# Optimization experiments

Hardware: AMD Instinct MI355X
Metric: run time of the kernel (lower is better)

## Reference

```python
import jax, jax.numpy as jnp
import numpy as np

B, IN, P, H, OUT = 131072, 40, 128, 256, 1

def setup_inputs() -> dict:
    key = jax.random.key(0)
    ks = jax.random.split(key, 10)
    s_in, s_h = 1.0 / np.sqrt(IN), 1.0 / np.sqrt(H)
    return {
        "x_step": jax.random.normal(ks[0], (B, 1, IN), jnp.float32),
        "hidden_in": jax.random.normal(ks[1], (1, B, H), jnp.float32),
        "W_proj": jax.random.uniform(ks[2], (P, IN), jnp.float32, -s_in, s_in),
        "b_proj": jax.random.uniform(ks[3], (P,), jnp.float32, -s_in, s_in),
        "W_ih": jax.random.uniform(ks[4], (3 * H, P), jnp.float32, -s_h, s_h),
        "W_hh": jax.random.uniform(ks[5], (3 * H, H), jnp.float32, -s_h, s_h),
        "b_ih": jax.random.uniform(ks[6], (3 * H,), jnp.float32, -s_h, s_h),
        "b_hh": jax.random.uniform(ks[7], (3 * H,), jnp.float32, -s_h, s_h),
        "W_head": jax.random.uniform(ks[8], (OUT, H), jnp.float32, -s_h, s_h),
        "b_head": jax.random.uniform(ks[9], (OUT,), jnp.float32, -s_h, s_h),
    }

def reference(x_step, hidden_in, W_proj, b_proj, W_ih, W_hh, b_ih, b_hh, W_head, b_head):
    # input projection: [B,1,IN] -> [B,P]
    x = jnp.einsum('bi,pi->bp', x_step[:, 0, :], W_proj) + b_proj
    h = hidden_in[0]  # [B,H]
    # single GRU step (PyTorch gate layout: reset, update, new)
    gi = jnp.einsum('bp,gp->bg', x, W_ih) + b_ih  # [B,3H]
    gh = jnp.einsum('bh,gh->bg', h, W_hh) + b_hh  # [B,3H]
    i_r, i_z, i_n = jnp.split(gi, 3, axis=-1)
    h_r, h_z, h_n = jnp.split(gh, 3, axis=-1)
    r = jax.nn.sigmoid(i_r + h_r)
    z = jax.nn.sigmoid(i_z + h_z)
    n = jnp.tanh(i_n + r * h_n)
    h_new = (1.0 - z) * n + z * h  # [B,H]
    pred = jnp.einsum('bh,oh->bo', h_new, W_head) + b_head  # [B,OUT]
    return pred[:, None, :], h_new[None]  # ([B,1,OUT], [1,B,H])
```

## Files before the change

kernel.cpp:

```cpp
#include <hip/hip_runtime.h>

#define B_N 131072
#define IN_N 40
#define H_N 256

typedef __bf16 bf16x8 __attribute__((ext_vector_type(8)));
typedef __bf16 bf16x4 __attribute__((ext_vector_type(4)));
typedef float f32x4 __attribute__((ext_vector_type(4)));

#define MFMA(a, b, c) __builtin_amdgcn_mfma_f32_16x16x32_bf16(a, b, c, 0, 0, 0)

#define WSF 0
#define WSH 49152
#define WSBI 245760
#define PREP_N (245760 + 768 + B_N)

__global__ void prep(const float* __restrict__ Wp, const float* __restrict__ bp,
                     const float* __restrict__ Wih, const float* __restrict__ Whh,
                     const float* __restrict__ bih, const float* __restrict__ bhead,
                     __bf16* __restrict__ wsb, float* __restrict__ out) {
  int i = blockIdx.x * 256 + threadIdx.x;
  if (i < WSH) {
    int g = i >> 6, kk = i & 63;
    float v = 0.f;
    if (kk < IN_N) {
      for (int p = 0; p < 128; ++p) v += Wih[g * 128 + p] * Wp[p * IN_N + kk];
    }
    wsb[i] = (__bf16)v;
  } else if (i < WSBI) {
    wsb[i] = (__bf16)Whh[i - WSH];
  } else if (i < WSBI + 768) {
    int g = i - WSBI;
    float v = bih[g];
    for (int p = 0; p < 128; ++p) v += Wih[g * 128 + p] * bp[p];
    ((float*)(wsb + WSBI))[g] = v;
  } else if (i < PREP_N) {
    out[i - (WSBI + 768)] = bhead[0];
  }
}

__global__ __launch_bounds__(512, 2) void gru_v6(
    const float* __restrict__ x, const float* __restrict__ h0,
    const __bf16* __restrict__ wsb, const float* __restrict__ bhh,
    const float* __restrict__ Whead, float* __restrict__ out) {
  __shared__ __bf16 hs[2][64][264];
  __shared__ __bf16 xs[2][64][72];

  const int tid = threadIdx.x;
  const int lane = tid & 63;
  const int w = tid >> 6;
  const int l15 = lane & 15;
  const int l4 = lane >> 4;
  const int koff = l4 * 8;

  const int b = blockIdx.x;
  const int v = (b & 7) * 64 + (b >> 3);
  const int half = v & 1;
  const int tile0 = (v >> 1) * 8;
  const int col = half * 128 + w * 16 + l15;

  const __bf16* WH = wsb + WSH;
  const __bf16* WF = wsb + WSF;
  bf16x8 whR[8], whZ[8], whN[8], wfR[2], wfZ[2], wfN[2];
#pragma unroll
  for (int ks = 0; ks < 8; ++ks) {
    const int k = ks * 32 + koff;
    whR[ks] = *reinterpret_cast<const bf16x8*>(WH + (size_t)col * 256 + k);
    whZ[ks] = *reinterpret_cast<const bf16x8*>(WH + (size_t)(256 + col) * 256 + k);
    whN[ks] = *reinterpret_cast<const bf16x8*>(WH + (size_t)(512 + col) * 256 + k);
  }
#pragma unroll
  for (int ks = 0; ks < 2; ++ks) {
    const int k = ks * 32 + koff;
    wfR[ks] = *reinterpret_cast<const bf16x8*>(WF + (size_t)col * 64 + k);
    wfZ[ks] = *reinterpret_cast<const bf16x8*>(WF + (size_t)(256 + col) * 64 + k);
    wfN[ks] = *reinterpret_cast<const bf16x8*>(WF + (size_t)(512 + col) * 64 + k);
  }
  const float* bfused = (const float*)(wsb + WSBI);
  const float bR = bfused[col] + bhh[col];
  const float bZ = bfused[256 + col] + bhh[256 + col];
  const float bI = bfused[512 + col];
  const float bH = bhh[512 + col];
  const float whead = Whead[col];

  auto stage = [&](int buf, int row0) {
    const float* hb = h0 + (size_t)row0 * H_N;
#pragma unroll
    for (int j = 0; j < 8; ++j) {
      const int flat = (tid + j * 512) * 4;
      const int r = flat >> 8, c = flat & 255;
      float4 vv = *reinterpret_cast<const float4*>(hb + flat);
      bf16x4 u;
      u[0] = (__bf16)vv.x; u[1] = (__bf16)vv.y; u[2] = (__bf16)vv.z; u[3] = (__bf16)vv.w;
      *reinterpret_cast<bf16x4*>(&hs[buf][r][c]) = u;
    }
    const float* xb = x + (size_t)row0 * IN_N;
#pragma unroll
    for (int j = 0; j < 5; ++j) {
      const int i = tid + j * 512;
      xs[buf][i / 40][i % 40] = (__bf16)xb[i];
    }
#pragma unroll
    for (int j = 0; j < 3; ++j) {
      const int i = tid + j * 512;
      xs[buf][i / 24][40 + i % 24] = (__bf16)0.f;
    }
  };

  stage(0, tile0 * 64);
  __syncthreads();

  for (int t = 0; t < 8; ++t) {
    const int cur = t & 1;
    const int row0 = (tile0 + t) * 64;
    if (t < 7) stage(cur ^ 1, row0 + 64);

    f32x4 aR[4], aZ[4], aI[4], aH[4];
#pragma unroll
    for (int mi = 0; mi < 4; ++mi) {
      aR[mi] = (f32x4){bR, bR, bR, bR};
      aZ[mi] = (f32x4){bZ, bZ, bZ, bZ};
      aI[mi] = (f32x4){bI, bI, bI, bI};
      aH[mi] = (f32x4){bH, bH, bH, bH};
    }
#pragma unroll
    for (int ks = 0; ks < 2; ++ks) {
#pragma unroll
      for (int mi = 0; mi < 4; ++mi) {
        const bf16x8 a = *reinterpret_cast<const bf16x8*>(&xs[cur][mi * 16 + l15][ks * 32 + koff]);
        aR[mi] = MFMA(a, wfR[ks], aR[mi]);
        aZ[mi] = MFMA(a, wfZ[ks], aZ[mi]);
        aI[mi] = MFMA(a, wfN[ks], aI[mi]);
      }
    }
#pragma unroll
    for (int ks = 0; ks < 8; ++ks) {
#pragma unroll
      for (int mi = 0; mi < 4; ++mi) {
        const bf16x8 a = *reinterpret_cast<const bf16x8*>(&hs[cur][mi * 16 + l15][ks * 32 + koff]);
        aR[mi] = MFMA(a, whR[ks], aR[mi]);
        aZ[mi] = MFMA(a, whZ[ks], aZ[mi]);
        aH[mi] = MFMA(a, whN[ks], aH[mi]);
      }
    }
    float ps[4][4];
#pragma unroll
    for (int mi = 0; mi < 4; ++mi) {
#pragma unroll
      for (int r = 0; r < 4; ++r) {
        const int row = mi * 16 + l4 * 4 + r;
        const float rg = 1.f / (1.f + __expf(-aR[mi][r]));
        const float zg = 1.f / (1.f + __expf(-aZ[mi][r]));
        const float e2 = __expf(2.f * (aI[mi][r] + rg * aH[mi][r]));
        const float ng = (e2 - 1.f) / (e2 + 1.f);
        const float hv = (float)hs[cur][row][col];
        const float hn = (1.f - zg) * ng + zg * hv;
        out[(size_t)B_N + (size_t)(row0 + row) * H_N + col] = hn;
        ps[mi][r] = hn * whead;
      }
    }
#pragma unroll
    for (int mi = 0; mi < 4; ++mi)
#pragma unroll
      for (int r = 0; r < 4; ++r) {
        float s = ps[mi][r];
        s += __shfl_xor(s, 1);
        s += __shfl_xor(s, 2);
        s += __shfl_xor(s, 4);
        s += __shfl_xor(s, 8);
        if (l15 == 0) atomicAdd(&out[row0 + mi * 16 + l4 * 4 + r], s);
      }
    __syncthreads();
  }
}

extern "C" void kernel_launch(void* const* d_in, const int* in_sizes, int n_in,
                              void* d_out, int out_size, void* d_ws, size_t ws_size,
                              hipStream_t stream) {
  const float* x     = (const float*)d_in[0];
  const float* h0    = (const float*)d_in[1];
  const float* Wp    = (const float*)d_in[2];
  const float* bp    = (const float*)d_in[3];
  const float* Wih   = (const float*)d_in[4];
  const float* Whh   = (const float*)d_in[5];
  const float* bih   = (const float*)d_in[6];
  const float* bhh   = (const float*)d_in[7];
  const float* Whead = (const float*)d_in[8];
  const float* bhead = (const float*)d_in[9];
  float* out = (float*)d_out;
  __bf16* wsb = (__bf16*)d_ws;

  prep<<<(PREP_N + 255) / 256, 256, 0, stream>>>(Wp, bp, Wih, Whh, bih, bhead, wsb, out);
  gru_v6<<<512, 512, 0, stream>>>(x, h0, wsb, bhh, Whead, out);
}
```

Before: 216.2 us.

## Stream weights from global per k-step and pipeline h loads with MFMA

Replaces register-resident gate weights with a pre-swizzled weight layout streamed from global memory in double-buffered slots, interleaved with MFMA groups. Block shape changes to 256 threads covering 64 output columns, with 1024 blocks. Staging of h/x is split into register loads and later LDS writes spread across the compute, and LDS uses an XOR swizzle instead of padding. Also uses rcp intrinsics for the gates and batches the atomics. The aim is to cut register pressure and hide global load latency behind compute, at the cost of re-reading weights from L2 each tile and sending more atomics per row, since four blocks now contribute to each row instead of two.

```diff
diff --git a/kernel.cpp b/kernel.cpp
--- a/kernel.cpp
+++ b/kernel.cpp
@@ -5,13 +5,12 @@
 #define H_N 256
 
 typedef __bf16 bf16x8 __attribute__((ext_vector_type(8)));
-typedef __bf16 bf16x4 __attribute__((ext_vector_type(4)));
 typedef float f32x4 __attribute__((ext_vector_type(4)));
 
 #define MFMA(a, b, c) __builtin_amdgcn_mfma_f32_16x16x32_bf16(a, b, c, 0, 0, 0)
 
-#define WSF 0
-#define WSH 49152
+#define WSGH 0
+#define WSGI 196608
 #define WSBI 245760
 #define PREP_N (245760 + 768 + B_N)
 
@@ -20,15 +19,18 @@
                      const float* __restrict__ bih, const float* __restrict__ bhead,
                      __bf16* __restrict__ wsb, float* __restrict__ out) {
   int i = blockIdx.x * 256 + threadIdx.x;
-  if (i < WSH) {
-    int g = i >> 6, kk = i & 63;
+  if (i < WSGI) {
+    int e = i & 31, col = (i >> 5) & 255, ks = (i >> 13) & 7, g = i >> 16;
+    wsb[i] = (__bf16)Whh[(g * 256 + col) * 256 + ks * 32 + e];
+  } else if (i < WSBI) {
+    int j = i - WSGI;
+    int e = j & 31, col = (j >> 5) & 255, ks2 = (j >> 13) & 1, g = j >> 14;
+    int k = ks2 * 32 + e;
     float v = 0.f;
-    if (kk < IN_N) {
-      for (int p = 0; p < 128; ++p) v += Wih[g * 128 + p] * Wp[p * IN_N + kk];
+    if (k < IN_N) {
+      for (int p = 0; p < 128; ++p) v += Wih[(g * 256 + col) * 128 + p] * Wp[p * IN_N + k];
     }
     wsb[i] = (__bf16)v;
-  } else if (i < WSBI) {
-    wsb[i] = (__bf16)Whh[i - WSH];
   } else if (i < WSBI + 768) {
     int g = i - WSBI;
     float v = bih[g];
@@ -39,43 +41,30 @@
   }
 }
 
-__global__ __launch_bounds__(512, 2) void gru_v6(
+__global__ __launch_bounds__(256, 2) void gru_v7(
     const float* __restrict__ x, const float* __restrict__ h0,
     const __bf16* __restrict__ wsb, const float* __restrict__ bhh,
     const float* __restrict__ Whead, float* __restrict__ out) {
-  __shared__ __bf16 hs[2][64][264];
-  __shared__ __bf16 xs[2][64][72];
+  __shared__ __align__(16) __bf16 hs[2][64 * 256];
+  __shared__ __align__(16) __bf16 xs[64][72];
 
   const int tid = threadIdx.x;
   const int lane = tid & 63;
   const int w = tid >> 6;
   const int l15 = lane & 15;
   const int l4 = lane >> 4;
-  const int koff = l4 * 8;
 
   const int b = blockIdx.x;
-  const int v = (b & 7) * 64 + (b >> 3);
-  const int half = v & 1;
-  const int tile0 = (v >> 1) * 8;
-  const int col = half * 128 + w * 16 + l15;
-
-  const __bf16* WH = wsb + WSH;
-  const __bf16* WF = wsb + WSF;
-  bf16x8 whR[8], whZ[8], whN[8], wfR[2], wfZ[2], wfN[2];
-#pragma unroll
-  for (int ks = 0; ks < 8; ++ks) {
-    const int k = ks * 32 + koff;
-    whR[ks] = *reinterpret_cast<const bf16x8*>(WH + (size_t)col * 256 + k);
-    whZ[ks] = *reinterpret_cast<const bf16x8*>(WH + (size_t)(256 + col) * 256 + k);
-    whN[ks] = *reinterpret_cast<const bf16x8*>(WH + (size_t)(512 + col) * 256 + k);
-  }
-#pragma unroll
-  for (int ks = 0; ks < 2; ++ks) {
-    const int k = ks * 32 + koff;
-    wfR[ks] = *reinterpret_cast<const bf16x8*>(WF + (size_t)col * 64 + k);
-    wfZ[ks] = *reinterpret_cast<const bf16x8*>(WF + (size_t)(256 + col) * 64 + k);
-    wfN[ks] = *reinterpret_cast<const bf16x8*>(WF + (size_t)(512 + col) * 64 + k);
-  }
+  const int lin = (b & 7) * 128 + (b >> 3);
+  const int ch = lin & 3;
+  const int seg0 = (lin >> 2) * 8;
+
+  const int cb = ch * 64 + w * 16;
+  const int col = cb + l15;
+
+  const __bf16* lgh = wsb + WSGH + (size_t)(cb + l15) * 32 + l4 * 8;
+  const __bf16* lgi = wsb + WSGI + (size_t)(cb + l15) * 32 + l4 * 8;
+
   const float* bfused = (const float*)(wsb + WSBI);
   const float bR = bfused[col] + bhh[col];
   const float bZ = bfused[256 + col] + bhh[256 + col];
@@ -83,79 +72,137 @@
   const float bH = bhh[512 + col];
   const float whead = Whead[col];
 
-  auto stage = [&](int buf, int row0) {
-    const float* hb = h0 + (size_t)row0 * H_N;
-#pragma unroll
-    for (int j = 0; j < 8; ++j) {
-      const int flat = (tid + j * 512) * 4;
-      const int r = flat >> 8, c = flat & 255;
-      float4 vv = *reinterpret_cast<const float4*>(hb + flat);
-      bf16x4 u;
-      u[0] = (__bf16)vv.x; u[1] = (__bf16)vv.y; u[2] = (__bf16)vv.z; u[3] = (__bf16)vv.w;
-      *reinterpret_cast<bf16x4*>(&hs[buf][r][c]) = u;
-    }
-    const float* xb = x + (size_t)row0 * IN_N;
-#pragma unroll
-    for (int j = 0; j < 5; ++j) {
-      const int i = tid + j * 512;
-      xs[buf][i / 40][i % 40] = (__bf16)xb[i];
-    }
-#pragma unroll
-    for (int j = 0; j < 3; ++j) {
-      const int i = tid + j * 512;
-      xs[buf][i / 24][40 + i % 24] = (__bf16)0.f;
-    }
-  };
-
-  stage(0, tile0 * 64);
+  for (int j = tid; j < 64 * 24; j += 256) xs[j / 24][40 + j % 24] = (__bf16)0.f;
+
+  float4 svA[4], svB[4], xv[4];
+
+  auto loadH = [&](float4(&sv)[4], int seg, int q) {
+#pragma unroll
+    for (int kk = 0; kk < 2; ++kk) {
+      const int cid = tid + kk * 256;
+      const int rl = q * 16 + (cid >> 5), ck = cid & 31;
+      const float* src = h0 + ((size_t)seg * 64 + rl) * H_N + ck * 8;
+      sv[kk * 2] = *reinterpret_cast<const float4*>(src);
+      sv[kk * 2 + 1] = *reinterpret_cast<const float4*>(src + 4);
+    }
+  };
+  auto writeH = [&](float4(&sv)[4], int buf, int q) {
+#pragma unroll
+    for (int kk = 0; kk < 2; ++kk) {
+      const int cid = tid + kk * 256;
+      const int rl = q * 16 + (cid >> 5), ck = cid & 31;
+      bf16x8 u;
+      u[0] = (__bf16)sv[kk * 2].x; u[1] = (__bf16)sv[kk * 2].y;
+      u[2] = (__bf16)sv[kk * 2].z; u[3] = (__bf16)sv[kk * 2].w;
+      u[4] = (__bf16)sv[kk * 2 + 1].x; u[5] = (__bf16)sv[kk * 2 + 1].y;
+      u[6] = (__bf16)sv[kk * 2 + 1].z; u[7] = (__bf16)sv[kk * 2 + 1].w;
+      *reinterpret_cast<bf16x8*>(&hs[buf][rl * 256 + ((ck ^ (rl & 7)) << 3)]) = u;
+    }
+  };
+  auto loadX = [&](int seg) {
+    const int c0 = tid, c1 = 256 + (tid & 63);
+    const float* sx = x + (size_t)seg * 64 * IN_N;
+    xv[0] = *reinterpret_cast<const float4*>(sx + c0 * 8);
+    xv[1] = *reinterpret_cast<const float4*>(sx + c0 * 8 + 4);
+    xv[2] = *reinterpret_cast<const float4*>(sx + c1 * 8);
+    xv[3] = *reinterpret_cast<const float4*>(sx + c1 * 8 + 4);
+  };
+  auto writeX = [&]() {
+    const int c0 = tid, c1 = 256 + (tid & 63);
+    bf16x8 u0, u1;
+    u0[0] = (__bf16)xv[0].x; u0[1] = (__bf16)xv[0].y; u0[2] = (__bf16)xv[0].z; u0[3] = (__bf16)xv[0].w;
+    u0[4] = (__bf16)xv[1].x; u0[5] = (__bf16)xv[1].y; u0[6] = (__bf16)xv[1].z; u0[7] = (__bf16)xv[1].w;
+    u1[0] = (__bf16)xv[2].x; u1[1] = (__bf16)xv[2].y; u1[2] = (__bf16)xv[2].z; u1[3] = (__bf16)xv[2].w;
+    u1[4] = (__bf16)xv[3].x; u1[5] = (__bf16)xv[3].y; u1[6] = (__bf16)xv[3].z; u1[7] = (__bf16)xv[3].w;
+    *reinterpret_cast<bf16x8*>(&xs[c0 / 5][(c0 % 5) * 8]) = u0;
+    *reinterpret_cast<bf16x8*>(&xs[c1 / 5][(c1 % 5) * 8]) = u1;
+  };
+
+  bf16x8 wR[2], wZ[2], wN[2];
+  auto loadWgrp = [&](int slot, int grp) {
+    if (grp < 2) {
+      wR[slot] = *reinterpret_cast<const bf16x8*>(lgi + (0 * 2 + grp) * 8192);
+      wZ[slot] = *reinterpret_cast<const bf16x8*>(lgi + (1 * 2 + grp) * 8192);
+      wN[slot] = *reinterpret_cast<const bf16x8*>(lgi + (2 * 2 + grp) * 8192);
+    } else {
+      const int ks = grp - 2;
+      wR[slot] = *reinterpret_cast<const bf16x8*>(lgh + (0 * 8 + ks) * 8192);
+      wZ[slot] = *reinterpret_cast<const bf16x8*>(lgh + (1 * 8 + ks) * 8192);
+      wN[slot] = *reinterpret_cast<const bf16x8*>(lgh + (2 * 8 + ks) * 8192);
+    }
+  };
+
+  f32x4 aR4[4], aZ4[4], aI4[4], aH4[4];
+  auto grpGI = [&](int slot, int ks2) {
+#pragma unroll
+    for (int mi = 0; mi < 4; ++mi) {
+      const bf16x8 a = *reinterpret_cast<const bf16x8*>(&xs[mi * 16 + l15][ks2 * 32 + l4 * 8]);
+      aR4[mi] = MFMA(a, wR[slot], aR4[mi]);
+      aZ4[mi] = MFMA(a, wZ[slot], aZ4[mi]);
+      aI4[mi] = MFMA(a, wN[slot], aI4[mi]);
+    }
+  };
+  auto grpGH = [&](const __bf16* hb, int slot, int ks) {
+#pragma unroll
+    for (int mi = 0; mi < 4; ++mi) {
+      const int row = mi * 16 + l15;
+      const int ck = (ks * 4 + l4) ^ (row & 7);
+      const bf16x8 a = *reinterpret_cast<const bf16x8*>(&hb[row * 256 + ck * 8]);
+      aR4[mi] = MFMA(a, wR[slot], aR4[mi]);
+      aZ4[mi] = MFMA(a, wZ[slot], aZ4[mi]);
+      aH4[mi] = MFMA(a, wN[slot], aH4[mi]);
+    }
+  };
+
+  loadH(svA, seg0, 0); writeH(svA, 0, 0);
+  loadH(svA, seg0, 1); writeH(svA, 0, 1);
+  loadH(svA, seg0, 2); writeH(svA, 0, 2);
+  loadH(svA, seg0, 3); writeH(svA, 0, 3);
+  loadX(seg0); writeX();
+  loadWgrp(0, 0); loadWgrp(1, 1);
   __syncthreads();
 
   for (int t = 0; t < 8; ++t) {
     const int cur = t & 1;
-    const int row0 = (tile0 + t) * 64;
-    if (t < 7) stage(cur ^ 1, row0 + 64);
-
-    f32x4 aR[4], aZ[4], aI[4], aH[4];
-#pragma unroll
-    for (int mi = 0; mi < 4; ++mi) {
-      aR[mi] = (f32x4){bR, bR, bR, bR};
-      aZ[mi] = (f32x4){bZ, bZ, bZ, bZ};
-      aI[mi] = (f32x4){bI, bI, bI, bI};
-      aH[mi] = (f32x4){bH, bH, bH, bH};
-    }
-#pragma unroll
-    for (int ks = 0; ks < 2; ++ks) {
-#pragma unroll
-      for (int mi = 0; mi < 4; ++mi) {
-        const bf16x8 a = *reinterpret_cast<const bf16x8*>(&xs[cur][mi * 16 + l15][ks * 32 + koff]);
-        aR[mi] = MFMA(a, wfR[ks], aR[mi]);
-        aZ[mi] = MFMA(a, wfZ[ks], aZ[mi]);
-        aI[mi] = MFMA(a, wfN[ks], aI[mi]);
-      }
-    }
-#pragma unroll
-    for (int ks = 0; ks < 8; ++ks) {
-#pragma unroll
-      for (int mi = 0; mi < 4; ++mi) {
-        const bf16x8 a = *reinterpret_cast<const bf16x8*>(&hs[cur][mi * 16 + l15][ks * 32 + koff]);
-        aR[mi] = MFMA(a, whR[ks], aR[mi]);
-        aZ[mi] = MFMA(a, whZ[ks], aZ[mi]);
-        aH[mi] = MFMA(a, whN[ks], aH[mi]);
-      }
-    }
+    const int seg = seg0 + t;
+    const int nseg = (t < 7) ? seg + 1 : seg;
+    const __bf16* hb = hs[cur];
+
+#pragma unroll
+    for (int mi = 0; mi < 4; ++mi) {
+      aR4[mi] = (f32x4){bR, bR, bR, bR};
+      aZ4[mi] = (f32x4){bZ, bZ, bZ, bZ};
+      aI4[mi] = (f32x4){bI, bI, bI, bI};
+      aH4[mi] = (f32x4){bH, bH, bH, bH};
+    }
+
+    grpGI(0, 0); loadWgrp(0, 2);
+    grpGI(1, 1); loadWgrp(1, 3);
+    __syncthreads();
+
+    grpGH(hb, 0, 0); loadWgrp(0, 4); loadH(svA, nseg, 0);
+    grpGH(hb, 1, 1); loadWgrp(1, 5); loadH(svB, nseg, 1);
+    grpGH(hb, 0, 2); loadWgrp(0, 6);
+    grpGH(hb, 1, 3); loadWgrp(1, 7); writeH(svA, cur ^ 1, 0); loadH(svA, nseg, 2);
+    grpGH(hb, 0, 4); loadWgrp(0, 8); writeH(svB, cur ^ 1, 1); loadH(svB, nseg, 3);
+    grpGH(hb, 1, 5); loadWgrp(1, 9); loadX(nseg);
+    grpGH(hb, 0, 6); loadWgrp(0, 0); writeH(svA, cur ^ 1, 2);
+    grpGH(hb, 1, 7); loadWgrp(1, 1); writeH(svB, cur ^ 1, 3); writeX();
+
     float ps[4][4];
 #pragma unroll
     for (int mi = 0; mi < 4; ++mi) {
 #pragma unroll
       for (int r = 0; r < 4; ++r) {
         const int row = mi * 16 + l4 * 4 + r;
-        const float rg = 1.f / (1.f + __expf(-aR[mi][r]));
-        const float zg = 1.f / (1.f + __expf(-aZ[mi][r]));
-        const float e2 = __expf(2.f * (aI[mi][r] + rg * aH[mi][r]));
-        const float ng = (e2 - 1.f) / (e2 + 1.f);
-        const float hv = (float)hs[cur][row][col];
+        const float rg = __builtin_amdgcn_rcpf(1.f + __expf(-aR4[mi][r]));
+        const float zg = __builtin_amdgcn_rcpf(1.f + __expf(-aZ4[mi][r]));
+        const float e2 = __expf(2.f * (aI4[mi][r] + rg * aH4[mi][r]));
+        const float ng = 1.f - 2.f * __builtin_amdgcn_rcpf(e2 + 1.f);
+        const int ckv = (col >> 3) ^ (row & 7);
+        const float hv = (float)hb[row * 256 + ckv * 8 + (col & 7)];
         const float hn = (1.f - zg) * ng + zg * hv;
-        out[(size_t)B_N + (size_t)(row0 + row) * H_N + col] = hn;
+        out[(size_t)B_N + ((size_t)seg * 64 + row) * H_N + col] = hn;
         ps[mi][r] = hn * whead;
       }
     }
@@ -168,8 +215,15 @@
         s += __shfl_xor(s, 2);
         s += __shfl_xor(s, 4);
         s += __shfl_xor(s, 8);
-        if (l15 == 0) atomicAdd(&out[row0 + mi * 16 + l4 * 4 + r], s);
+        ps[mi][r] = s;
       }
+    if (l15 == 0) {
+#pragma unroll
+      for (int mi = 0; mi < 4; ++mi)
+#pragma unroll
+        for (int r = 0; r < 4; ++r)
+          atomicAdd(&out[seg * 64 + mi * 16 + l4 * 4 + r], ps[mi][r]);
+    }
     __syncthreads();
   }
 }
@@ -191,5 +245,5 @@
   __bf16* wsb = (__bf16*)d_ws;
 
   prep<<<(PREP_N + 255) / 256, 256, 0, stream>>>(Wp, bp, Wih, Whh, bih, bhead, wsb, out);
-  gru_v6<<<512, 512, 0, stream>>>(x, h0, wsb, bhh, Whead, out);
+  gru_v7<<<1024, 256, 0, stream>>>(x, h0, wsb, bhh, Whead, out);
 }
```

Result: slower. 284.1 us (+31.4%).

## Replace persistent register-resident weight kernel with many small blocks streaming fragment-packed weights

Applied to the files above, without the earlier changes.

Drops the persistent kernel that held weights in registers and looped over eight double-buffered 64-row tiles per block. The new kernel launches 8192 blocks of 256 threads; each handles one 64-row batch tile and a quarter of the hidden columns, loading weight fragments from a prepacked, coalesced layout built by the prep kernel. It relies on block-level parallelism and occupancy instead of in-block pipelining. Each h/x row tile is now staged four times (once per column quarter), and weights are re-read from L2 by every block.

```diff
diff --git a/kernel.cpp b/kernel.cpp
--- a/kernel.cpp
+++ b/kernel.cpp
@@ -5,13 +5,12 @@
 #define H_N 256
 
 typedef __bf16 bf16x8 __attribute__((ext_vector_type(8)));
-typedef __bf16 bf16x4 __attribute__((ext_vector_type(4)));
 typedef float f32x4 __attribute__((ext_vector_type(4)));
 
 #define MFMA(a, b, c) __builtin_amdgcn_mfma_f32_16x16x32_bf16(a, b, c, 0, 0, 0)
 
-#define WSF 0
-#define WSH 49152
+#define WSGH 0
+#define WSGI 196608
 #define WSBI 245760
 #define PREP_N (245760 + 768 + B_N)
 
@@ -20,15 +19,18 @@
                      const float* __restrict__ bih, const float* __restrict__ bhead,
                      __bf16* __restrict__ wsb, float* __restrict__ out) {
   int i = blockIdx.x * 256 + threadIdx.x;
-  if (i < WSH) {
-    int g = i >> 6, kk = i & 63;
+  if (i < WSGI) {
+    int e = i & 31, col = (i >> 5) & 255, ks = (i >> 13) & 7, g = i >> 16;
+    wsb[i] = (__bf16)Whh[(g * 256 + col) * 256 + ks * 32 + e];
+  } else if (i < WSBI) {
+    int j = i - WSGI;
+    int e = j & 31, col = (j >> 5) & 255, ks2 = (j >> 13) & 1, g = j >> 14;
+    int k = ks2 * 32 + e;
     float v = 0.f;
-    if (kk < IN_N) {
-      for (int p = 0; p < 128; ++p) v += Wih[g * 128 + p] * Wp[p * IN_N + kk];
+    if (k < IN_N) {
+      for (int p = 0; p < 128; ++p) v += Wih[(g * 256 + col) * 128 + p] * Wp[p * IN_N + k];
     }
     wsb[i] = (__bf16)v;
-  } else if (i < WSBI) {
-    wsb[i] = (__bf16)Whh[i - WSH];
   } else if (i < WSBI + 768) {
     int g = i - WSBI;
     float v = bih[g];
@@ -39,12 +41,12 @@
   }
 }
 
-__global__ __launch_bounds__(512, 2) void gru_v6(
+__global__ __launch_bounds__(256, 3) void gru_v8(
     const float* __restrict__ x, const float* __restrict__ h0,
     const __bf16* __restrict__ wsb, const float* __restrict__ bhh,
     const float* __restrict__ Whead, float* __restrict__ out) {
-  __shared__ __bf16 hs[2][64][264];
-  __shared__ __bf16 xs[2][64][72];
+  __shared__ __align__(16) __bf16 hs[64][264];
+  __shared__ __align__(16) __bf16 xs[64][72];
 
   const int tid = threadIdx.x;
   const int lane = tid & 63;
@@ -53,29 +55,42 @@
   const int l4 = lane >> 4;
   const int koff = l4 * 8;
 
-  const int b = blockIdx.x;
-  const int v = (b & 7) * 64 + (b >> 3);
-  const int half = v & 1;
-  const int tile0 = (v >> 1) * 8;
-  const int col = half * 128 + w * 16 + l15;
+  const int lin = (blockIdx.x & 7) * 1024 + (blockIdx.x >> 3);
+  const int ch = lin & 3;
+  const int b0 = (lin >> 2) * 64;
+  const int col = ch * 64 + w * 16 + l15;
 
-  const __bf16* WH = wsb + WSH;
-  const __bf16* WF = wsb + WSF;
-  bf16x8 whR[8], whZ[8], whN[8], wfR[2], wfZ[2], wfN[2];
+  for (int j = tid; j < 64 * 24; j += 256) xs[j / 24][40 + j % 24] = (__bf16)0.f;
 #pragma unroll
-  for (int ks = 0; ks < 8; ++ks) {
-    const int k = ks * 32 + koff;
-    whR[ks] = *reinterpret_cast<const bf16x8*>(WH + (size_t)col * 256 + k);
-    whZ[ks] = *reinterpret_cast<const bf16x8*>(WH + (size_t)(256 + col) * 256 + k);
-    whN[ks] = *reinterpret_cast<const bf16x8*>(WH + (size_t)(512 + col) * 256 + k);
+  for (int j = 0; j < 2; ++j) {
+    const int cid = tid + j * 256;
+    if (cid < 320) {
+      const int r = cid / 5, cc = cid % 5;
+      const float* s = x + (size_t)(b0 + r) * IN_N + cc * 8;
+      const float4 a = *reinterpret_cast<const float4*>(s);
+      const float4 b = *reinterpret_cast<const float4*>(s + 4);
+      bf16x8 u;
+      u[0] = (__bf16)a.x; u[1] = (__bf16)a.y; u[2] = (__bf16)a.z; u[3] = (__bf16)a.w;
+      u[4] = (__bf16)b.x; u[5] = (__bf16)b.y; u[6] = (__bf16)b.z; u[7] = (__bf16)b.w;
+      *reinterpret_cast<bf16x8*>(&xs[r][cc * 8]) = u;
+    }
   }
 #pragma unroll
-  for (int ks = 0; ks < 2; ++ks) {
-    const int k = ks * 32 + koff;
-    wfR[ks] = *reinterpret_cast<const bf16x8*>(WF + (size_t)col * 64 + k);
-    wfZ[ks] = *reinterpret_cast<const bf16x8*>(WF + (size_t)(256 + col) * 64 + k);
-    wfN[ks] = *reinterpret_cast<const bf16x8*>(WF + (size_t)(512 + col) * 64 + k);
+  for (int j = 0; j < 8; ++j) {
+    const int cid = tid + j * 256;
+    const int r = cid >> 5, cc = cid & 31;
+    const float* s = h0 + (size_t)(b0 + r) * H_N + cc * 8;
+    const float4 a = *reinterpret_cast<const float4*>(s);
+    const float4 b = *reinterpret_cast<const float4*>(s + 4);
+    bf16x8 u;
+    u[0] = (__bf16)a.x; u[1] = (__bf16)a.y; u[2] = (__bf16)a.z; u[3] = (__bf16)a.w;
+    u[4] = (__bf16)b.x; u[5] = (__bf16)b.y; u[6] = (__bf16)b.z; u[7] = (__bf16)b.w;
+    *reinterpret_cast<bf16x8*>(&hs[r][cc * 8]) = u;
   }
+  __syncthreads();
+
+  const __bf16* lgh = wsb + WSGH + (size_t)col * 32 + koff;
+  const __bf16* lgi = wsb + WSGI + (size_t)col * 32 + koff;
   const float* bfused = (const float*)(wsb + WSBI);
   const float bR = bfused[col] + bhh[col];
   const float bZ = bfused[256 + col] + bhh[256 + col];
@@ -83,95 +98,69 @@
   const float bH = bhh[512 + col];
   const float whead = Whead[col];
 
-  auto stage = [&](int buf, int row0) {
-    const float* hb = h0 + (size_t)row0 * H_N;
+  f32x4 aR[4], aZ[4], aI[4], aH[4];
 #pragma unroll
-    for (int j = 0; j < 8; ++j) {
-      const int flat = (tid + j * 512) * 4;
-      const int r = flat >> 8, c = flat & 255;
-      float4 vv = *reinterpret_cast<const float4*>(hb + flat);
-      bf16x4 u;
-      u[0] = (__bf16)vv.x; u[1] = (__bf16)vv.y; u[2] = (__bf16)vv.z; u[3] = (__bf16)vv.w;
-      *reinterpret_cast<bf16x4*>(&hs[buf][r][c]) = u;
-    }
-    const float* xb = x + (size_t)row0 * IN_N;
+  for (int mi = 0; mi < 4; ++mi) {
+    aR[mi] = (f32x4){bR, bR, bR, bR};
+    aZ[mi] = (f32x4){bZ, bZ, bZ, bZ};
+    aI[mi] = (f32x4){bI, bI, bI, bI};
+    aH[mi] = (f32x4){bH, bH, bH, bH};
+  }
+
 #pragma unroll
-    for (int j = 0; j < 5; ++j) {
-      const int i = tid + j * 512;
-      xs[buf][i / 40][i % 40] = (__bf16)xb[i];
-    }
-#pragma unroll
-    for (int j = 0; j < 3; ++j) {
-      const int i = tid + j * 512;
-      xs[buf][i / 24][40 + i % 24] = (__bf16)0.f;
-    }
-  };
-
-  stage(0, tile0 * 64);
-  __syncthreads();
-
-  for (int t = 0; t < 8; ++t) {
-    const int cur = t & 1;
-    const int row0 = (tile0 + t) * 64;
-    if (t < 7) stage(cur ^ 1, row0 + 64);
-
-    f32x4 aR[4], aZ[4], aI[4], aH[4];
+  for (int ks = 0; ks < 2; ++ks) {
+    const bf16x8 wR = *reinterpret_cast<const bf16x8*>(lgi + (0 * 2 + ks) * 8192);
+    const bf16x8 wZ = *reinterpret_cast<const bf16x8*>(lgi + (1 * 2 + ks) * 8192);
+    const bf16x8 wN = *reinterpret_cast<const bf16x8*>(lgi + (2 * 2 + ks) * 8192);
 #pragma unroll
     for (int mi = 0; mi < 4; ++mi) {
-      aR[mi] = (f32x4){bR, bR, bR, bR};
-      aZ[mi] = (f32x4){bZ, bZ, bZ, bZ};
-      aI[mi] = (f32x4){bI, bI, bI, bI};
-      aH[mi] = (f32x4){bH, bH, bH, bH};
+      const bf16x8 a = *reinterpret_cast<const bf16x8*>(&xs[mi * 16 + l15][ks * 32 + koff]);
+      aR[mi] = MFMA(a, wR, aR[mi]);
+      aZ[mi] = MFMA(a, wZ, aZ[mi]);
+      aI[mi] = MFMA(a, wN, aI[mi]);
     }
+  }
 #pragma unroll
-    for (int ks = 0; ks < 2; ++ks) {
-#pragma unroll
-      for (int mi = 0; mi < 4; ++mi) {
-        const bf16x8 a = *reinterpret_cast<const bf16x8*>(&xs[cur][mi * 16 + l15][ks * 32 + koff]);
-        aR[mi] = MFMA(a, wfR[ks], aR[mi]);
-        aZ[mi] = MFMA(a, wfZ[ks], aZ[mi]);
-        aI[mi] = MFMA(a, wfN[ks], aI[mi]);
-      }
-    }
-#pragma unroll
-    for (int ks = 0; ks < 8; ++ks) {
-#pragma unroll
-      for (int mi = 0; mi < 4; ++mi) {
-        const bf16x8 a = *reinterpret_cast<const bf16x8*>(&hs[cur][mi * 16 + l15][ks * 32 + koff]);
-        aR[mi] = MFMA(a, whR[ks], aR[mi]);
-        aZ[mi] = MFMA(a, whZ[ks], aZ[mi]);
-        aH[mi] = MFMA(a, whN[ks], aH[mi]);
-      }
-    }
-    float ps[4][4];
+  for (int ks = 0; ks < 8; ++ks) {
+    const bf16x8 wR = *reinterpret_cast<const bf16x8*>(lgh + (0 * 8 + ks) * 8192);
+    const bf16x8 wZ = *reinterpret_cast<const bf16x8*>(lgh + (1 * 8 + ks) * 8192);
+    const bf16x8 wN = *reinterpret_cast<const bf16x8*>(lgh + (2 * 8 + ks) * 8192);
 #pragma unroll
     for (int mi = 0; mi < 4; ++mi) {
+      const bf16x8 a = *reinterpret_cast<const bf16x8*>(&hs[mi * 16 + l15][ks * 32 + koff]);
+      aR[mi] = MFMA(a, wR, aR[mi]);
+      aZ[mi] = MFMA(a, wZ, aZ[mi]);
+      aH[mi] = MFMA(a, wN, aH[mi]);
+    }
+  }
+
+  float ps[4][4];
 #pragma unroll
-      for (int r = 0; r < 4; ++r) {
-        const int row = mi * 16 + l4 * 4 + r;
-        const float rg = 1.f / (1.f + __expf(-aR[mi][r]));
-        const float zg = 1.f / (1.f + __expf(-aZ[mi][r]));
-        const float e2 = __expf(2.f * (aI[mi][r] + rg * aH[mi][r]));
-        const float ng = (e2 - 1.f) / (e2 + 1.f);
-        const float hv = (float)hs[cur][row][col];
-        const float hn = (1.f - zg) * ng + zg * hv;
-        out[(size_t)B_N + (size_t)(row0 + row) * H_N + col] = hn;
-        ps[mi][r] = hn * whead;
-      }
+  for (int mi = 0; mi < 4; ++mi) {
+#pragma unroll
+    for (int r = 0; r < 4; ++r) {
+      const int row = mi * 16 + l4 * 4 + r;
+      const float rg = 1.f / (1.f + __expf(-aR[mi][r]));
+      const float zg = 1.f / (1.f + __expf(-aZ[mi][r]));
+      const float e2 = __expf(2.f * (aI[mi][r] + rg * aH[mi][r]));
+      const float ng = (e2 - 1.f) / (e2 + 1.f);
+      const float hv = (float)hs[row][col];
+      const float hn = (1.f - zg) * ng + zg * hv;
+      out[(size_t)B_N + (size_t)(b0 + row) * H_N + col] = hn;
+      ps[mi][r] = hn * whead;
     }
+  }
 #pragma unroll
-    for (int mi = 0; mi < 4; ++mi)
+  for (int mi = 0; mi < 4; ++mi)
 #pragma unroll
-      for (int r = 0; r < 4; ++r) {
-        float s = ps[mi][r];
-        s += __shfl_xor(s, 1);
-        s += __shfl_xor(s, 2);
-        s += __shfl_xor(s, 4);
-        s += __shfl_xor(s, 8);
-        if (l15 == 0) atomicAdd(&out[row0 + mi * 16 + l4 * 4 + r], s);
-      }
-    __syncthreads();
-  }
+    for (int r = 0; r < 4; ++r) {
+      float s = ps[mi][r];
+      s += __shfl_xor(s, 1);
+      s += __shfl_xor(s, 2);
+      s += __shfl_xor(s, 4);
+      s += __shfl_xor(s, 8);
+      if (l15 == 0) atomicAdd(&out[b0 + mi * 16 + l4 * 4 + r], s);
+    }
 }
 
 extern "C" void kernel_launch(void* const* d_in, const int* in_sizes, int n_in,
@@ -191,5 +180,5 @@
   __bf16* wsb = (__bf16*)d_ws;
 
   prep<<<(PREP_N + 255) / 256, 256, 0, stream>>>(Wp, bp, Wih, Whh, bih, bhead, wsb, out);
-  gru_v6<<<512, 512, 0, stream>>>(x, h0, wsb, bhh, Whead, out);
+  gru_v8<<<8192, 256, 0, stream>>>(x, h0, wsb, bhh, Whead, out);
 }
```

Result: slower. 251.9 us (+16.5%).

## Prefetch next tile into registers during MFMA and relayout weights for coalescing

Applied to the files above, without the earlier changes.

The next tile's h and x loads are now issued into registers before the MFMA loop and written to shared memory after it, so global latency overlaps the matrix math instead of stalling ahead of it. Prep now stores the weights in a ks-major, column-interleaved layout so each lane's weight fragment loads are contiguous across lanes. The zero padding of xs is written once up front rather than every iteration, and launch bounds drop from 2 to 1 blocks per SM. The larger register footprint from prefetching and the lower occupancy hint could reduce latency hiding.

```diff
diff --git a/kernel.cpp b/kernel.cpp
--- a/kernel.cpp
+++ b/kernel.cpp
@@ -10,8 +10,8 @@
 
 #define MFMA(a, b, c) __builtin_amdgcn_mfma_f32_16x16x32_bf16(a, b, c, 0, 0, 0)
 
-#define WSF 0
-#define WSH 49152
+#define WSGH 0
+#define WSGI 196608
 #define WSBI 245760
 #define PREP_N (245760 + 768 + B_N)
 
@@ -20,15 +20,18 @@
                      const float* __restrict__ bih, const float* __restrict__ bhead,
                      __bf16* __restrict__ wsb, float* __restrict__ out) {
   int i = blockIdx.x * 256 + threadIdx.x;
-  if (i < WSH) {
-    int g = i >> 6, kk = i & 63;
+  if (i < WSGI) {
+    int e = i & 31, col = (i >> 5) & 255, ks = (i >> 13) & 7, g = i >> 16;
+    wsb[i] = (__bf16)Whh[(g * 256 + col) * 256 + ks * 32 + e];
+  } else if (i < WSBI) {
+    int j = i - WSGI;
+    int e = j & 31, col = (j >> 5) & 255, ks2 = (j >> 13) & 1, g = j >> 14;
+    int k = ks2 * 32 + e;
     float v = 0.f;
-    if (kk < IN_N) {
-      for (int p = 0; p < 128; ++p) v += Wih[g * 128 + p] * Wp[p * IN_N + kk];
+    if (k < IN_N) {
+      for (int p = 0; p < 128; ++p) v += Wih[(g * 256 + col) * 128 + p] * Wp[p * IN_N + k];
     }
     wsb[i] = (__bf16)v;
-  } else if (i < WSBI) {
-    wsb[i] = (__bf16)Whh[i - WSH];
   } else if (i < WSBI + 768) {
     int g = i - WSBI;
     float v = bih[g];
@@ -39,7 +42,7 @@
   }
 }
 
-__global__ __launch_bounds__(512, 2) void gru_v6(
+__global__ __launch_bounds__(512, 1) void gru_v9(
     const float* __restrict__ x, const float* __restrict__ h0,
     const __bf16* __restrict__ wsb, const float* __restrict__ bhh,
     const float* __restrict__ Whead, float* __restrict__ out) {
@@ -53,28 +56,26 @@
   const int l4 = lane >> 4;
   const int koff = l4 * 8;
 
-  const int b = blockIdx.x;
-  const int v = (b & 7) * 64 + (b >> 3);
-  const int half = v & 1;
-  const int tile0 = (v >> 1) * 8;
+  const int lin = (blockIdx.x & 7) * 64 + (blockIdx.x >> 3);
+  const int half = lin & 1;
+  const int seg0 = (lin >> 1) * 8;
   const int col = half * 128 + w * 16 + l15;
 
-  const __bf16* WH = wsb + WSH;
-  const __bf16* WF = wsb + WSF;
-  bf16x8 whR[8], whZ[8], whN[8], wfR[2], wfZ[2], wfN[2];
+  const __bf16* lgh = wsb + WSGH + (size_t)col * 32 + koff;
+  const __bf16* lgi = wsb + WSGI + (size_t)col * 32 + koff;
+  bf16x8 whR[8], whZ[8], whN[8];
 #pragma unroll
   for (int ks = 0; ks < 8; ++ks) {
-    const int k = ks * 32 + koff;
-    whR[ks] = *reinterpret_cast<const bf16x8*>(WH + (size_t)col * 256 + k);
-    whZ[ks] = *reinterpret_cast<const bf16x8*>(WH + (size_t)(256 + col) * 256 + k);
-    whN[ks] = *reinterpret_cast<const bf16x8*>(WH + (size_t)(512 + col) * 256 + k);
-  }
+    whR[ks] = *reinterpret_cast<const bf16x8*>(lgh + (0 * 8 + ks) * 8192);
+    whZ[ks] = *reinterpret_cast<const bf16x8*>(lgh + (1 * 8 + ks) * 8192);
+    whN[ks] = *reinterpret_cast<const bf16x8*>(lgh + (2 * 8 + ks) * 8192);
+  }
+  bf16x8 wfR[2], wfZ[2], wfN[2];
 #pragma unroll
   for (int ks = 0; ks < 2; ++ks) {
-    const int k = ks * 32 + koff;
-    wfR[ks] = *reinterpret_cast<const bf16x8*>(WF + (size_t)col * 64 + k);
-    wfZ[ks] = *reinterpret_cast<const bf16x8*>(WF + (size_t)(256 + col) * 64 + k);
-    wfN[ks] = *reinterpret_cast<const bf16x8*>(WF + (size_t)(512 + col) * 64 + k);
+    wfR[ks] = *reinterpret_cast<const bf16x8*>(lgi + (0 * 2 + ks) * 8192);
+    wfZ[ks] = *reinterpret_cast<const bf16x8*>(lgi + (1 * 2 + ks) * 8192);
+    wfN[ks] = *reinterpret_cast<const bf16x8*>(lgi + (2 * 2 + ks) * 8192);
   }
   const float* bfused = (const float*)(wsb + WSBI);
   const float bR = bfused[col] + bhh[col];
@@ -83,37 +84,45 @@
   const float bH = bhh[512 + col];
   const float whead = Whead[col];
 
-  auto stage = [&](int buf, int row0) {
-    const float* hb = h0 + (size_t)row0 * H_N;
+  for (int j = tid; j < 2 * 64 * 24; j += 512) {
+    const int bb = j / (64 * 24), jj = j % (64 * 24);
+    xs[bb][jj / 24][40 + jj % 24] = (__bf16)0.f;
+  }
+
+  {
+    const float* hb = h0 + (size_t)seg0 * 64 * H_N;
 #pragma unroll
     for (int j = 0; j < 8; ++j) {
-      const int flat = (tid + j * 512) * 4;
-      const int r = flat >> 8, c = flat & 255;
-      float4 vv = *reinterpret_cast<const float4*>(hb + flat);
+      const int cid = tid + j * 512;
+      const float4 v = *reinterpret_cast<const float4*>(hb + (size_t)cid * 4);
       bf16x4 u;
-      u[0] = (__bf16)vv.x; u[1] = (__bf16)vv.y; u[2] = (__bf16)vv.z; u[3] = (__bf16)vv.w;
-      *reinterpret_cast<bf16x4*>(&hs[buf][r][c]) = u;
-    }
-    const float* xb = x + (size_t)row0 * IN_N;
+      u[0] = (__bf16)v.x; u[1] = (__bf16)v.y; u[2] = (__bf16)v.z; u[3] = (__bf16)v.w;
+      *reinterpret_cast<bf16x4*>(&hs[0][cid >> 6][(cid & 63) * 4]) = u;
+    }
+    const float* xb = x + (size_t)seg0 * 64 * IN_N;
 #pragma unroll
     for (int j = 0; j < 5; ++j) {
       const int i = tid + j * 512;
-      xs[buf][i / 40][i % 40] = (__bf16)xb[i];
-    }
-#pragma unroll
-    for (int j = 0; j < 3; ++j) {
-      const int i = tid + j * 512;
-      xs[buf][i / 24][40 + i % 24] = (__bf16)0.f;
-    }
-  };
-
-  stage(0, tile0 * 64);
+      xs[0][i / 40][i % 40] = (__bf16)xb[i];
+    }
+  }
   __syncthreads();
 
   for (int t = 0; t < 8; ++t) {
     const int cur = t & 1;
-    const int row0 = (tile0 + t) * 64;
-    if (t < 7) stage(cur ^ 1, row0 + 64);
+    const int seg = seg0 + t;
+
+    float4 sv[8];
+    float sx[5];
+    if (t < 7) {
+      const float* hb = h0 + (size_t)(seg + 1) * 64 * H_N;
+#pragma unroll
+      for (int j = 0; j < 8; ++j)
+        sv[j] = *reinterpret_cast<const float4*>(hb + (size_t)(tid + j * 512) * 4);
+      const float* xb = x + (size_t)(seg + 1) * 64 * IN_N;
+#pragma unroll
+      for (int j = 0; j < 5; ++j) sx[j] = xb[tid + j * 512];
+    }
 
     f32x4 aR[4], aZ[4], aI[4], aH[4];
 #pragma unroll
@@ -124,7 +133,7 @@
       aH[mi] = (f32x4){bH, bH, bH, bH};
     }
 #pragma unroll
-    for (int ks = 0; ks < 2; ++ks) {
+    for (int ks = 0; ks < 2; ++ks)
 #pragma unroll
       for (int mi = 0; mi < 4; ++mi) {
         const bf16x8 a = *reinterpret_cast<const bf16x8*>(&xs[cur][mi * 16 + l15][ks * 32 + koff]);
@@ -132,9 +141,8 @@
         aZ[mi] = MFMA(a, wfZ[ks], aZ[mi]);
         aI[mi] = MFMA(a, wfN[ks], aI[mi]);
       }
-    }
-#pragma unroll
-    for (int ks = 0; ks < 8; ++ks) {
+#pragma unroll
+    for (int ks = 0; ks < 8; ++ks)
 #pragma unroll
       for (int mi = 0; mi < 4; ++mi) {
         const bf16x8 a = *reinterpret_cast<const bf16x8*>(&hs[cur][mi * 16 + l15][ks * 32 + koff]);
@@ -142,7 +150,23 @@
         aZ[mi] = MFMA(a, whZ[ks], aZ[mi]);
         aH[mi] = MFMA(a, whN[ks], aH[mi]);
       }
-    }
+
+    if (t < 7) {
+#pragma unroll
+      for (int j = 0; j < 8; ++j) {
+        const int cid = tid + j * 512;
+        bf16x4 u;
+        u[0] = (__bf16)sv[j].x; u[1] = (__bf16)sv[j].y;
+        u[2] = (__bf16)sv[j].z; u[3] = (__bf16)sv[j].w;
+        *reinterpret_cast<bf16x4*>(&hs[cur ^ 1][cid >> 6][(cid & 63) * 4]) = u;
+      }
+#pragma unroll
+      for (int j = 0; j < 5; ++j) {
+        const int i = tid + j * 512;
+        xs[cur ^ 1][i / 40][i % 40] = (__bf16)sx[j];
+      }
+    }
+
     float ps[4][4];
 #pragma unroll
     for (int mi = 0; mi < 4; ++mi) {
@@ -155,7 +179,7 @@
         const float ng = (e2 - 1.f) / (e2 + 1.f);
         const float hv = (float)hs[cur][row][col];
         const float hn = (1.f - zg) * ng + zg * hv;
-        out[(size_t)B_N + (size_t)(row0 + row) * H_N + col] = hn;
+        out[(size_t)B_N + ((size_t)seg * 64 + row) * H_N + col] = hn;
         ps[mi][r] = hn * whead;
       }
     }
@@ -168,7 +192,7 @@
         s += __shfl_xor(s, 2);
         s += __shfl_xor(s, 4);
         s += __shfl_xor(s, 8);
-        if (l15 == 0) atomicAdd(&out[row0 + mi * 16 + l4 * 4 + r], s);
+        if (l15 == 0) atomicAdd(&out[seg * 64 + mi * 16 + l4 * 4 + r], s);
       }
     __syncthreads();
   }
@@ -191,5 +215,5 @@
   __bf16* wsb = (__bf16*)d_ws;
 
   prep<<<(PREP_N + 255) / 256, 256, 0, stream>>>(Wp, bp, Wih, Whh, bih, bhead, wsb, out);
-  gru_v6<<<512, 512, 0, stream>>>(x, h0, wsb, bhh, Whead, out);
+  gru_v9<<<512, 512, 0, stream>>>(x, h0, wsb, bhh, Whead, out);
 }
```

Result: slower. 328.7 us (+52.1%).
